# Performance work log

Hardware: AMD Instinct MI355X
Metric: run time of the kernel (lower is better)

## Reference

```python
import jax, jax.numpy as jnp
import numpy as np

B, S, H, TRK = 128, 256, 300, 64  # batch, seq tokens, hidden size, tracker size
N_STEPS = 2 * S - 1


def _valid_transitions(rng, batch, n_tok):
    """Random valid shift(0)/reduce(1) sequences of length 2*n_tok-1."""
    out = np.zeros((batch, 2 * n_tok - 1), dtype=np.int32)
    for b in range(batch):
        shifts_left, depth = n_tok, 0
        for i in range(2 * n_tok - 1):
            if depth < 2:
                a = 0
            elif shifts_left == 0:
                a = 1
            else:
                a = int(rng.integers(0, 2))
            out[b, i] = a
            if a == 0:
                shifts_left -= 1
                depth += 1
            else:
                depth -= 1
    return out


def setup_inputs() -> dict:
    key = jax.random.key(0)
    ks = jax.random.split(key, 12)
    sh = 1.0 / np.sqrt(H)
    st = 1.0 / np.sqrt(TRK)
    bufs = jax.random.normal(ks[0], (B, S, 2 * H), dtype=jnp.float32)
    transitions = jnp.asarray(_valid_transitions(np.random.default_rng(0), B, S))
    return {
        "bufs": bufs,
        "transitions": transitions,
        # tracker bundling projections (bias=False): Linear(size, 4*tracker)
        "W_buf": jax.random.uniform(ks[1], (H, 4 * TRK), jnp.float32, -sh, sh),
        "W_s1": jax.random.uniform(ks[2], (H, 4 * TRK), jnp.float32, -sh, sh),
        "W_s2": jax.random.uniform(ks[3], (H, 4 * TRK), jnp.float32, -sh, sh),
        # tracker LSTMCell(4*TRK, TRK, bias=False)
        "W_ih": jax.random.uniform(ks[4], (4 * TRK, 4 * TRK), jnp.float32, -st, st),
        "W_hh": jax.random.uniform(ks[5], (4 * TRK, TRK), jnp.float32, -st, st),
        # transition predictor Linear(TRK, 2)
        "W_trans": jax.random.uniform(ks[6], (TRK, 2), jnp.float32, -st, st),
        "b_trans": jax.random.uniform(ks[7], (2,), jnp.float32, -st, st),
        # Reduce (TreeLSTM composition, 5*H gates) with tracking input
        "W_left": jax.random.uniform(ks[8], (H, 5 * H), jnp.float32, -sh, sh),
        "W_right": jax.random.uniform(ks[9], (H, 5 * H), jnp.float32, -sh, sh),
        "W_track": jax.random.uniform(ks[10], (TRK, 5 * H), jnp.float32, -st, st),
        "b_reduce": jax.random.uniform(ks[11], (5 * H,), jnp.float32, -sh, sh),
    }


def reference(bufs, transitions, W_buf, W_s1, W_s2, W_ih, W_hh,
              W_trans, b_trans, W_left, W_right, W_track, b_reduce):
    Bn, Sn, D = bufs.shape
    Hn = D // 2  # element = concat(h, c)
    Tn = W_hh.shape[1]
    bidx = jnp.arange(Bn)

    stack0 = jnp.zeros((Bn, Sn + 1, D), dtype=bufs.dtype)
    carry0 = (stack0,
              jnp.zeros((Bn,), jnp.int32),          # stack ptr
              jnp.zeros((Bn,), jnp.int32),          # buffer ptr
              jnp.zeros((Bn, Tn), bufs.dtype),       # tracker h
              jnp.zeros((Bn, Tn), bufs.dtype))       # tracker c

    def gather(stack, ptr, off):
        el = stack[bidx, jnp.clip(ptr - off, 0)]
        return jnp.where((ptr >= off)[:, None], el, jnp.zeros_like(el))

    def step(carry, trans):
        stack, sptr, bptr, th, tc = carry
        buf_top = bufs[bidx, jnp.clip(bptr, 0, Sn - 1)]   # [B, 2H]
        s1 = gather(stack, sptr, 1)                        # stack[-1]
        s2 = gather(stack, sptr, 2)                        # stack[-2]
        # bundle h-parts -> tracker LSTM input (sum of three projections)
        lstm_in = buf_top[:, :Hn] @ W_buf + s1[:, :Hn] @ W_s1 + s2[:, :Hn] @ W_s2
        gates = lstm_in @ W_ih.T + th @ W_hh.T             # [B, 4T]
        gi, gf, gg, go = jnp.split(gates, 4, axis=1)       # torch LSTMCell order i,f,g,o
        tc = jax.nn.sigmoid(gf) * tc + jax.nn.sigmoid(gi) * jnp.tanh(gg)
        th = jax.nn.sigmoid(go) * jnp.tanh(tc)
        logits = th @ W_trans + b_trans                    # [B, 2]
        # TreeLSTM reduce: left = stack[-2], right = stack[-1]
        a = s2[:, :Hn] @ W_left + s1[:, :Hn] @ W_right + th @ W_track + b_reduce
        ri, fl, fr, ro, rg = jnp.split(a, 5, axis=1)
        rc = (jax.nn.sigmoid(fl) * s2[:, Hn:] + jax.nn.sigmoid(fr) * s1[:, Hn:]
              + jax.nn.sigmoid(ri) * jnp.tanh(rg))
        rh = jax.nn.sigmoid(ro) * jnp.tanh(rc)
        reduced = jnp.concatenate([rh, rc], axis=1)
        is_shift = (trans == 0)
        new_el = jnp.where(is_shift[:, None], buf_top, reduced)
        wpos = jnp.where(is_shift, sptr, jnp.clip(sptr - 2, 0))
        stack = stack.at[bidx, wpos].set(new_el)
        sptr = jnp.where(is_shift, sptr + 1, sptr - 1)
        bptr = bptr + is_shift.astype(jnp.int32)
        return (stack, sptr, bptr, th, tc), logits

    (stack, sptr, _, _, _), logits = jax.lax.scan(step, carry0, transitions.T)
    final_h = stack[bidx, jnp.clip(sptr - 1, 0)][:, :Hn]   # [B, H]
    # pack sentence encoding + per-step transition logits into one array
    return jnp.concatenate(
        [final_h, logits.transpose(1, 0, 2).reshape(Bn, -1)], axis=1)
```

## Files before the change

### kernel.cpp

```cpp
#include <hip/hip_runtime.h>


#define NSTEP 511
#define HB 128
#define SQ 256
#define HD 300
#define DW 600
#define TK 64

#define NB 16
#define NE 25
#define JPB 12
#define DOTS_E 60
#define KE 640
#define UPB 10
#define DOTS_T 40
#define KT2 1000
#define ASTR 20
#define SLP 820
#define OUTW 1322

#define N_WEB 960000
#define N_WTB 280000
#define N_WTR 97500
#define N_TH  16384
#define N_STACK 19660800
#define N_BAR 1024
#define N_TPK 4096
#define N_WCT 230400

#define OFF_WEB 0
#define OFF_WTB 960000
#define OFF_WTR 1240000
#define OFF_TH  1337504
#define OFF_STACK 1353888
#define OFF_BAR 21014688
#define OFF_TPK 21015712
#define WS_FLOATS 21019808
#define OFF_WCT OFF_STACK

#define L_ACT 0
#define L_DUMP 20500
#define EDP 964
#define TDP 644
#define L_WTR 28212
#define L_THL 32112
#define L_BRED 33152
#define L_TRW 36600
#define L_INT 37112
#define LDS_FLOATS 37208

__device__ __forceinline__ float sigf(float x) { return 1.0f / (1.0f + __expf(-x)); }

__global__ void prep_a(const float* __restrict__ Wbuf, const float* __restrict__ Ws1,
                       const float* __restrict__ Ws2, const int* __restrict__ trans,
                       float* __restrict__ ws) {
  int idx = blockIdx.x * 256 + threadIdx.x;
  if (idx < N_WCT) {
    int k = idx % 900;
    int m = idx / 900;
    float v = (k < 300) ? Wbuf[k*256 + m]
            : (k < 600) ? Ws1[(k-300)*256 + m]
                        : Ws2[(k-600)*256 + m];
    ws[OFF_WCT + idx] = v;
    return;
  }
  idx -= N_WCT;
  if (idx < N_TH) { ws[OFF_TH + idx] = 0.0f; return; }
  idx -= N_TH;
  if (idx < N_BAR) { ws[OFF_BAR + idx] = 0.0f; return; }
  idx -= N_BAR;
  if (idx < 8*NSTEP) {
    int g = idx / NSTEP, t = idx % NSTEP;
    int w = 0;
    #pragma unroll
    for (int b = 0; b < 16; ++b)
      w |= (trans[(size_t)(g*16 + b)*NSTEP + t] & 1) << b;
    ((int*)(ws + OFF_TPK))[g*NSTEP + t] = w;
  }
}

__global__ void prep_b(const float* __restrict__ Wih, const float* __restrict__ Whh,
                       const float* __restrict__ Wl, const float* __restrict__ Wr,
                       const float* __restrict__ Wtrk, float* __restrict__ ws) {
  int idx = blockIdx.x * 256 + threadIdx.x;
  if (idx < N_WEB) {
    int k = idx % KE; int rest = idx / KE;
    int dot = rest % DOTS_E; int e = rest / DOTS_E;
    int g = dot / JPB, jj = dot % JPB;
    int col = g*HD + e*JPB + jj;
    float v = 0.0f;
    if (k < 300)      v = Wl[k*1500 + col];
    else if (k < 600) v = Wr[(k-300)*1500 + col];
    ws[OFF_WEB + idx] = v;
    return;
  }
  idx -= N_WEB;
  if (idx < N_WTB) {
    int k = idx % KT2; int rest = idx / KT2;
    int dot = rest % DOTS_T; int tb = rest / DOTS_T;
    int g = dot / UPB, uu = dot % UPB;
    int ucnt = (tb == 6) ? 10 : 9;
    float v = 0.0f;
    if (uu < ucnt) {
      int col = g*TK + tb*9 + uu;
      if (k < 900) {
        const float* wct = ws + OFF_WCT;
        const float* wi  = Wih + col*256;
        float s = 0.0f;
        #pragma unroll 4
        for (int m = 0; m < 256; ++m) s = fmaf(wct[m*900 + k], wi[m], s);
        v = s;
      } else if (k < 964) {
        v = Whh[col*TK + (k - 900)];
      }
    }
    ws[OFF_WTB + idx] = v;
    return;
  }
  idx -= N_WTB;
  if (idx < N_WTR) {
    int k = idx % 65; int rest = idx / 65;
    int dot = rest % DOTS_E; int e = rest / DOTS_E;
    int g = dot / JPB, jj = dot % JPB;
    ws[OFF_WTR + idx] = (k < 64) ? Wtrk[k*1500 + (g*HD + e*JPB + jj)] : 0.0f;
  }
}

__device__ __forceinline__ void xbar(int role, unsigned epoch,
                                     volatile unsigned* slots, volatile unsigned* flag,
                                     volatile int* broken) {
  __syncthreads();
  if (role == 0) {
    if (threadIdx.x < 64) {
      int lane = threadIdx.x;
      unsigned spins = 0;
      for (;;) {
        if (*broken) break;
        unsigned v = (lane >= 1 && lane < 32) ? slots[lane] : epoch;
        if (__all(v >= epoch)) break;
        __builtin_amdgcn_s_sleep(1);
        asm volatile("buffer_inv" ::: "memory");
        if (++spins > 2000000u) { if (lane == 0) *broken = 1; break; }
      }
      if (lane == 0) {
        *flag = epoch;
        asm volatile("s_waitcnt vmcnt(0)" ::: "memory");
      }
    }
  } else if (threadIdx.x == 0) {
    slots[role] = epoch;
    asm volatile("s_waitcnt vmcnt(0)" ::: "memory");
    unsigned spins = 0;
    while (!*broken && *flag < epoch) {
      __builtin_amdgcn_s_sleep(1);
      asm volatile("buffer_inv" ::: "memory");
      if (++spins > 2000000u) *broken = 1;
    }
  }
  __syncthreads();
  asm volatile("buffer_inv" ::: "memory");
}

__launch_bounds__(256, 1)
__global__ void spinn_kernel(const float* __restrict__ bufs,
                             const float* __restrict__ Wtrans, const float* __restrict__ btrans,
                             const float* __restrict__ bredv,
                             float* __restrict__ ws, float* __restrict__ out) {
  extern __shared__ float lds[];
  int* ibuf = (int*)(lds + L_INT);
  int* redl = ibuf + 16;
  int* shl  = ibuf + 32;
  int* sptr = ibuf + 48;
  int* bptr = ibuf + 64;
  volatile int* broken = ibuf + 82;
  int* role_s = ibuf + 90;
  int* trw = (int*)(lds + L_TRW);

  const int tid = threadIdx.x;

  unsigned xcc;
  asm volatile("s_getreg_b32 %0, hwreg(HW_REG_XCC_ID)" : "=s"(xcc));
  xcc &= 7u;
  if (tid == 0) {
    unsigned slot = __hip_atomic_fetch_add((unsigned*)(ws + OFF_BAR) + 512 + xcc, 1u,
                                           __ATOMIC_RELAXED, __HIP_MEMORY_SCOPE_AGENT);
    *role_s = (int)slot;
    *broken = 0;
  }
  __syncthreads();
  const int role = *role_s;
  const int group = (int)xcc;
  if (role >= 32) return;

  const int b0 = group * NB;
  const bool isE = (role < NE);
  const int e  = role;
  const int tb = role - NE;
  const int u0 = (tb >= 0) ? tb*9 : 0;
  const int ucnt = (tb == 6) ? 10 : 9;

  volatile unsigned* slots = (volatile unsigned*)((unsigned*)(ws + OFF_BAR) + (size_t)group*64);
  volatile unsigned* flag  = slots + 32;

  float* stack = ws + OFF_STACK;
  float* thbuf = ws + OFF_TH;

  float tc_reg = 0.0f;

  float4 wreg[4][10];
  if (isE) {
    if (tid < 240) {
      const int q = tid >> 4, kq = tid & 15;
      const float* wb = ws + OFF_WEB;
      #pragma unroll
      for (int d = 0; d < 4; ++d)
        #pragma unroll
        for (int i = 0; i < 10; ++i)
          wreg[d][i] = *(const float4*)(wb + (size_t)(e*DOTS_E + 4*q + d)*KE + kq*40 + 4*i);
    }
  } else {
    if (tid < 250) {
      const int q = tid / 25, kq = tid % 25;
      const float* wb = ws + OFF_WTB;
      #pragma unroll
      for (int d = 0; d < 4; ++d)
        #pragma unroll
        for (int i = 0; i < 10; ++i)
          wreg[d][i] = *(const float4*)(wb + (size_t)(tb*DOTS_T + 4*q + d)*KT2 + kq*40 + 4*i);
    }
  }

  if (tid < 16) { sptr[tid] = 0; bptr[tid] = 0; }
  for (int i = tid; i < NSTEP; i += 256)
    trw[i] = ((const int*)(ws + OFF_TPK))[group*NSTEP + i];
  if (isE) {
    for (int i = tid; i < DOTS_E*65; i += 256)
      lds[L_WTR + i] = ws[OFF_WTR + (size_t)e*DOTS_E*65 + i];
    for (int i = tid; i < DOTS_E; i += 256)
      lds[L_BRED + i] = bredv[(i/JPB)*HD + e*JPB + (i%JPB)];
    for (int i = tid; i < 800; i += 256) lds[615*ASTR + i] = 0.0f;
  } else {
    for (int i = tid; i < 720; i += 256) lds[988*ASTR + i] = 0.0f;
  }
  __syncthreads();

  unsigned epoch = 0;

  for (int t = 0; t < NSTEP; ++t) {
    const int w = trw[t] & 0xFFFF;
    const int nred = __popc(w);
    if (tid < 16) {
      int rank = __popc(w & ((1u << tid) - 1u));
      if ((w >> tid) & 1) redl[rank] = tid; else shl[tid - rank] = tid;
    }
    __syncthreads();

    if (isE) {
      int r = tid >> 4, lane = tid & 15;
      if (r < nred) {
        int b = redl[r];
        int sp = sptr[b];
        const float* s2p = stack + ((size_t)((b0+b)*SQ + sp-2))*DW;
        const float* s1p = stack + ((size_t)((b0+b)*SQ + sp-1))*DW;
        #pragma unroll 4
        for (int i = 0; i < 10; ++i) {
          int ch = lane + 16*i;
          if (ch < 150) {
            int sec = ch / 75, kc = ch % 75;
            int dim = kc*4;
            const float* src = (sec == 0) ? s2p : s1p;
            float4 v = *(const float4*)(src + dim);
            int kbase = sec*300 + dim;
            int row0 = (kbase/40)*41 + (kbase%40);
            lds[(row0+0)*ASTR + r] = v.x;
            lds[(row0+1)*ASTR + r] = v.y;
            lds[(row0+2)*ASTR + r] = v.z;
            lds[(row0+3)*ASTR + r] = v.w;
          }
        }
      }
    } else {
      {
        int b = tid >> 4, lane = tid & 15;
        int bp = bptr[b]; if (bp > SQ-1) bp = SQ-1;
        int sp = sptr[b];
        const float* bsrc = bufs + ((size_t)((b0+b)*SQ + bp))*DW;
        const float* s1p = (sp >= 1) ? stack + ((size_t)((b0+b)*SQ + sp-1))*DW : nullptr;
        const float* s2p = (sp >= 2) ? stack + ((size_t)((b0+b)*SQ + sp-2))*DW : nullptr;
        #pragma unroll 4
        for (int i = 0; i < 15; ++i) {
          int ch = lane + 16*i;
          if (ch < 225) {
            int sec = ch / 75, kc = ch % 75;
            int dim = kc*4;
            const float* src = (sec == 0) ? bsrc : ((sec == 1) ? s1p : s2p);
            float4 v = make_float4(0.f, 0.f, 0.f, 0.f);
            if (src) v = *(const float4*)(src + dim);
            int kbase = sec*300 + dim;
            int row0 = (kbase/40)*41 + (kbase%40);
            lds[(row0+0)*ASTR + b] = v.x;
            lds[(row0+1)*ASTR + b] = v.y;
            lds[(row0+2)*ASTR + b] = v.z;
            lds[(row0+3)*ASTR + b] = v.w;
          }
        }
      }
      {
        int pm = (t - 1) & 1;
        int b = tid >> 4, uc = tid & 15;
        float4 v = *(const float4*)(thbuf + ((size_t)pm*HB + (b0+b))*TK + uc*4);
        float vv[4] = {v.x, v.y, v.z, v.w};
        #pragma unroll
        for (int l = 0; l < 4; ++l) {
          int k = 900 + uc*4 + l;
          int row = (k/40)*41 + (k%40);
          lds[row*ASTR + b] = vv[l];
        }
      }
    }
    __syncthreads();

    if (isE) {
      const int nchunk = (nred + 3) >> 2;
      if (nchunk > 0) {
        if (tid < 240) {
          const int q = tid >> 4, kq = tid & 15;
          const float* ab = lds + kq*SLP;
          float* dmp = lds + L_DUMP;
          #pragma unroll 1
          for (int c = 0; c < nchunk; ++c) {
            float acc[4][4];
            #pragma unroll
            for (int d = 0; d < 4; ++d)
              #pragma unroll
              for (int s = 0; s < 4; ++s) acc[d][s] = 0.0f;
            #pragma unroll
            for (int i = 0; i < 10; ++i) {
              #pragma unroll
              for (int kk = 0; kk < 4; ++kk) {
                float4 a = *(const float4*)(ab + (4*i + kk)*ASTR + 4*c);
                #pragma unroll
                for (int d = 0; d < 4; ++d) {
                  float wv = (kk == 0) ? wreg[d][i].x : (kk == 1) ? wreg[d][i].y
                           : (kk == 2) ? wreg[d][i].z : wreg[d][i].w;
                  acc[d][0] = fmaf(wv, a.x, acc[d][0]);
                  acc[d][1] = fmaf(wv, a.y, acc[d][1]);
                  acc[d][2] = fmaf(wv, a.z, acc[d][2]);
                  acc[d][3] = fmaf(wv, a.w, acc[d][3]);
                }
              }
            }
            #pragma unroll
            for (int d = 0; d < 4; ++d)
              #pragma unroll
              for (int s = 0; s < 4; ++s)
                acc[d][s] += __shfl_xor(acc[d][s], 8, 64);
            if (kq < 8) {
              #pragma unroll
              for (int d = 0; d < 4; ++d)
                *(float4*)(dmp + kq*EDP + (4*q + d)*16 + 4*c) =
                    make_float4(acc[d][0], acc[d][1], acc[d][2], acc[d][3]);
            }
          }
        }
        __syncthreads();
        for (int task = tid; task < DOTS_E*16; task += 256) {
          int dot = task >> 4, s = task & 15;
          float sum = 0.0f;
          #pragma unroll
          for (int kq = 0; kq < 8; ++kq)
            sum += lds[L_DUMP + kq*EDP + dot*16 + s];
          lds[L_DUMP + dot*16 + s] = sum;
        }
      }
    } else {
      if (tid < 250) {
        const int q = tid / 25, kq = tid % 25;
        const float* ab = lds + kq*SLP;
        float* dmp = lds + L_DUMP + kq*TDP;
        #pragma unroll 1
        for (int c = 0; c < 4; ++c) {
          float acc[4][4];
          #pragma unroll
          for (int d = 0; d < 4; ++d)
            #pragma unroll
            for (int s = 0; s < 4; ++s) acc[d][s] = 0.0f;
          #pragma unroll
          for (int i = 0; i < 10; ++i) {
            #pragma unroll
            for (int kk = 0; kk < 4; ++kk) {
              float4 a = *(const float4*)(ab + (4*i + kk)*ASTR + 4*c);
              #pragma unroll
              for (int d = 0; d < 4; ++d) {
                float wv = (kk == 0) ? wreg[d][i].x : (kk == 1) ? wreg[d][i].y
                         : (kk == 2) ? wreg[d][i].z : wreg[d][i].w;
                acc[d][0] = fmaf(wv, a.x, acc[d][0]);
                acc[d][1] = fmaf(wv, a.y, acc[d][1]);
                acc[d][2] = fmaf(wv, a.z, acc[d][2]);
                acc[d][3] = fmaf(wv, a.w, acc[d][3]);
              }
            }
          }
          #pragma unroll
          for (int d = 0; d < 4; ++d)
            *(float4*)(dmp + (4*q + d)*16 + 4*c) =
                make_float4(acc[d][0], acc[d][1], acc[d][2], acc[d][3]);
        }
      }
      __syncthreads();
      for (int task = tid; task < DOTS_T*16; task += 256) {
        int dot = task >> 4, s = task & 15;
        float sum = 0.0f;
        #pragma unroll
        for (int kq = 0; kq < 25; ++kq)
          sum += lds[L_DUMP + kq*TDP + dot*16 + s];
        lds[L_DUMP + dot*16 + s] = sum;
      }
      __syncthreads();
      if (tid < 160) {
        int uu = tid >> 4, b = tid & 15;
        if (uu < ucnt) {
          float gi = lds[L_DUMP + (0*UPB + uu)*16 + b];
          float gf = lds[L_DUMP + (1*UPB + uu)*16 + b];
          float gg = lds[L_DUMP + (2*UPB + uu)*16 + b];
          float go = lds[L_DUMP + (3*UPB + uu)*16 + b];
          tc_reg = sigf(gf)*tc_reg + sigf(gi)*tanhf(gg);
          float th = sigf(go)*tanhf(tc_reg);
          thbuf[((size_t)(t & 1)*HB + (b0 + b))*TK + (u0 + uu)] = th;
        }
      }
    }

    ++epoch;
    xbar(role, epoch, slots, flag, broken);

    if (isE) {
      int p = t & 1;
      {
        int r = tid >> 4, lane = tid & 15;
        if (r < nred) {
          const float* thp = thbuf + ((size_t)p*HB + (b0 + redl[r]))*TK;
          #pragma unroll
          for (int i = 0; i < 4; ++i) {
            int k = lane + 16*i;
            lds[L_THL + r*65 + k] = thp[k];
          }
        }
      }
      __syncthreads();
      if (tid < 192) {
        int rr = tid / JPB, jj = tid % JPB;
        int j = e*JPB + jj;
        if (rr < nred) {
          int b = redl[rr];
          int sp = sptr[b];
          float* s2base = stack + ((size_t)((b0+b)*SQ + (sp-2)))*DW;
          const float* s1base = stack + ((size_t)((b0+b)*SQ + (sp-1)))*DW;
          float s2c = s2base[HD + j];
          float s1c = s1base[HD + j];
          float a0 = lds[L_DUMP + (0*JPB + jj)*16 + rr] + lds[L_BRED + 0*JPB + jj];
          float a1 = lds[L_DUMP + (1*JPB + jj)*16 + rr] + lds[L_BRED + 1*JPB + jj];
          float a2 = lds[L_DUMP + (2*JPB + jj)*16 + rr] + lds[L_BRED + 2*JPB + jj];
          float a3 = lds[L_DUMP + (3*JPB + jj)*16 + rr] + lds[L_BRED + 3*JPB + jj];
          float a4 = lds[L_DUMP + (4*JPB + jj)*16 + rr] + lds[L_BRED + 4*JPB + jj];
          #pragma unroll 8
          for (int k = 0; k < 64; ++k) {
            float tv = lds[L_THL + rr*65 + k];
            a0 = fmaf(tv, lds[L_WTR + (0*JPB + jj)*65 + k], a0);
            a1 = fmaf(tv, lds[L_WTR + (1*JPB + jj)*65 + k], a1);
            a2 = fmaf(tv, lds[L_WTR + (2*JPB + jj)*65 + k], a2);
            a3 = fmaf(tv, lds[L_WTR + (3*JPB + jj)*65 + k], a3);
            a4 = fmaf(tv, lds[L_WTR + (4*JPB + jj)*65 + k], a4);
          }
          float rc = sigf(a1)*s2c + sigf(a2)*s1c + sigf(a0)*tanhf(a4);
          float rh = sigf(a3)*tanhf(rc);
          s2base[j] = rh;
          s2base[HD + j] = rc;
        } else {
          int b = shl[rr - nred];
          int sp = sptr[b], bp = bptr[b];
          const float* src = bufs + ((size_t)((b0+b)*SQ + bp))*DW;
          float* dst = stack + ((size_t)((b0+b)*SQ + sp))*DW;
          dst[j] = src[j];
          dst[HD + j] = src[HD + j];
        }
      }
    } else if (role == NE) {
      if (tid < 32) {
        int b = tid >> 1, c = tid & 1;
        const float* th = thbuf + ((size_t)(t & 1)*HB + (b0 + b))*TK;
        float s = btrans[c];
        #pragma unroll 8
        for (int u = 0; u < TK; ++u) s = fmaf(th[u], Wtrans[u*2 + c], s);
        out[(size_t)(b0 + b)*OUTW + HD + 2*t + c] = s;
      }
    }

    __syncthreads();
    if (tid < 16) {
      if (!((w >> tid) & 1)) { sptr[tid] += 1; bptr[tid] += 1; }
      else                   { sptr[tid] -= 1; }
    }

    ++epoch;
    xbar(role, epoch, slots, flag, broken);
  }

  if (isE && tid < 192) {
    int b = tid / JPB, jj = tid % JPB;
    int j = e*JPB + jj;
    int sp = sptr[b] - 1; if (sp < 0) sp = 0;
    out[(size_t)(b0 + b)*OUTW + j] =
        stack[((size_t)((b0 + b)*SQ + sp))*DW + j];
  }
}

extern "C" void kernel_launch(void* const* d_in, const int* in_sizes, int n_in,
                              void* d_out, int out_size, void* d_ws, size_t ws_size,
                              hipStream_t stream) {
  const float* bufs   = (const float*)d_in[0];
  const int*   trans  = (const int*)  d_in[1];
  const float* Wbuf   = (const float*)d_in[2];
  const float* Ws1    = (const float*)d_in[3];
  const float* Ws2    = (const float*)d_in[4];
  const float* Wih    = (const float*)d_in[5];
  const float* Whh    = (const float*)d_in[6];
  const float* Wtrans = (const float*)d_in[7];
  const float* btrans = (const float*)d_in[8];
  const float* Wl     = (const float*)d_in[9];
  const float* Wr     = (const float*)d_in[10];
  const float* Wtrk   = (const float*)d_in[11];
  const float* bredv  = (const float*)d_in[12];
  float* ws  = (float*)d_ws;
  float* out = (float*)d_out;

  if (ws_size < (size_t)WS_FLOATS * sizeof(float)) return;

  {
    int total = N_WCT + N_TH + N_BAR + 8*NSTEP;
    prep_a<<<(total + 255) / 256, 256, 0, stream>>>(Wbuf, Ws1, Ws2, trans, ws);
  }
  {
    int total = N_WEB + N_WTB + N_WTR;
    prep_b<<<(total + 255) / 256, 256, 0, stream>>>(Wih, Whh, Wl, Wr, Wtrk, ws);
  }
  (void)hipFuncSetAttribute((const void*)spinn_kernel,
                            hipFuncAttributeMaxDynamicSharedMemorySize, 160000);
  spinn_kernel<<<256, 256, LDS_FLOATS * sizeof(float), stream>>>(
      bufs, Wtrans, btrans, bredv, ws, out);
}
```

Baseline: 13.02 ms.

## Quadruple threads per block and spread dot products across more lanes

Raises the block size from 256 to 1024 threads. Each thread now holds one weight row slice instead of four, so the per-step matvec has four times the threads, each running a shorter dependency chain with fewer registers. The tracker-input reduction in the reduce phase is split across four lanes with shuffle reductions, and the staging loads use wider lanes. The aim is lower per-step latency in this latency-bound recurrent loop, at the cost of more wavefronts in each __syncthreads and the cross-block barrier, and the launch-bounds change affects register allocation.

```diff
diff --git a/kernel.cpp b/kernel.cpp
--- a/kernel.cpp
+++ b/kernel.cpp
@@ -162,7 +162,7 @@
   asm volatile("buffer_inv" ::: "memory");
 }
 
-__launch_bounds__(256, 1)
+__launch_bounds__(1024, 4)
 __global__ void spinn_kernel(const float* __restrict__ bufs,
                              const float* __restrict__ Wtrans, const float* __restrict__ btrans,
                              const float* __restrict__ bredv,
@@ -208,40 +208,34 @@
 
   float tc_reg = 0.0f;
 
-  float4 wreg[4][10];
+  float4 wreg[10];
   if (isE) {
-    if (tid < 240) {
+    if (tid < 960) {
       const int q = tid >> 4, kq = tid & 15;
-      const float* wb = ws + OFF_WEB;
+      const float* wb = ws + OFF_WEB + (size_t)(e*DOTS_E + q)*KE + kq*40;
       #pragma unroll
-      for (int d = 0; d < 4; ++d)
-        #pragma unroll
-        for (int i = 0; i < 10; ++i)
-          wreg[d][i] = *(const float4*)(wb + (size_t)(e*DOTS_E + 4*q + d)*KE + kq*40 + 4*i);
+      for (int i = 0; i < 10; ++i) wreg[i] = *(const float4*)(wb + 4*i);
     }
   } else {
-    if (tid < 250) {
+    if (tid < 1000) {
       const int q = tid / 25, kq = tid % 25;
-      const float* wb = ws + OFF_WTB;
+      const float* wb = ws + OFF_WTB + (size_t)(tb*DOTS_T + q)*KT2 + kq*40;
       #pragma unroll
-      for (int d = 0; d < 4; ++d)
-        #pragma unroll
-        for (int i = 0; i < 10; ++i)
-          wreg[d][i] = *(const float4*)(wb + (size_t)(tb*DOTS_T + 4*q + d)*KT2 + kq*40 + 4*i);
+      for (int i = 0; i < 10; ++i) wreg[i] = *(const float4*)(wb + 4*i);
     }
   }
 
   if (tid < 16) { sptr[tid] = 0; bptr[tid] = 0; }
-  for (int i = tid; i < NSTEP; i += 256)
+  for (int i = tid; i < NSTEP; i += 1024)
     trw[i] = ((const int*)(ws + OFF_TPK))[group*NSTEP + i];
   if (isE) {
-    for (int i = tid; i < DOTS_E*65; i += 256)
+    for (int i = tid; i < DOTS_E*65; i += 1024)
       lds[L_WTR + i] = ws[OFF_WTR + (size_t)e*DOTS_E*65 + i];
-    for (int i = tid; i < DOTS_E; i += 256)
+    for (int i = tid; i < DOTS_E; i += 1024)
       lds[L_BRED + i] = bredv[(i/JPB)*HD + e*JPB + (i%JPB)];
-    for (int i = tid; i < 800; i += 256) lds[615*ASTR + i] = 0.0f;
+    for (int i = tid; i < 800; i += 1024) lds[615*ASTR + i] = 0.0f;
   } else {
-    for (int i = tid; i < 720; i += 256) lds[988*ASTR + i] = 0.0f;
+    for (int i = tid; i < 720; i += 1024) lds[988*ASTR + i] = 0.0f;
   }
   __syncthreads();
 
@@ -257,15 +251,15 @@
     __syncthreads();
 
     if (isE) {
-      int r = tid >> 4, lane = tid & 15;
+      int r = tid >> 6, lane = tid & 63;
       if (r < nred) {
         int b = redl[r];
         int sp = sptr[b];
         const float* s2p = stack + ((size_t)((b0+b)*SQ + sp-2))*DW;
         const float* s1p = stack + ((size_t)((b0+b)*SQ + sp-1))*DW;
-        #pragma unroll 4
-        for (int i = 0; i < 10; ++i) {
-          int ch = lane + 16*i;
+        #pragma unroll
+        for (int i = 0; i < 3; ++i) {
+          int ch = lane + 64*i;
           if (ch < 150) {
             int sec = ch / 75, kc = ch % 75;
             int dim = kc*4;
@@ -282,15 +276,15 @@
       }
     } else {
       {
-        int b = tid >> 4, lane = tid & 15;
+        int b = tid >> 6, lane = tid & 63;
         int bp = bptr[b]; if (bp > SQ-1) bp = SQ-1;
         int sp = sptr[b];
         const float* bsrc = bufs + ((size_t)((b0+b)*SQ + bp))*DW;
         const float* s1p = (sp >= 1) ? stack + ((size_t)((b0+b)*SQ + sp-1))*DW : nullptr;
         const float* s2p = (sp >= 2) ? stack + ((size_t)((b0+b)*SQ + sp-2))*DW : nullptr;
-        #pragma unroll 4
-        for (int i = 0; i < 15; ++i) {
-          int ch = lane + 16*i;
+        #pragma unroll
+        for (int i = 0; i < 4; ++i) {
+          int ch = lane + 64*i;
           if (ch < 225) {
             int sec = ch / 75, kc = ch % 75;
             int dim = kc*4;
@@ -306,7 +300,7 @@
           }
         }
       }
-      {
+      if (tid < 256) {
         int pm = (t - 1) & 1;
         int b = tid >> 4, uc = tid & 15;
         float4 v = *(const float4*)(thbuf + ((size_t)pm*HB + (b0+b))*TK + uc*4);
@@ -324,48 +318,36 @@
     if (isE) {
       const int nchunk = (nred + 3) >> 2;
       if (nchunk > 0) {
-        if (tid < 240) {
+        if (tid < 960) {
           const int q = tid >> 4, kq = tid & 15;
           const float* ab = lds + kq*SLP;
           float* dmp = lds + L_DUMP;
           #pragma unroll 1
           for (int c = 0; c < nchunk; ++c) {
-            float acc[4][4];
-            #pragma unroll
-            for (int d = 0; d < 4; ++d)
-              #pragma unroll
-              for (int s = 0; s < 4; ++s) acc[d][s] = 0.0f;
+            float a0 = 0.f, a1 = 0.f, a2 = 0.f, a3 = 0.f;
             #pragma unroll
             for (int i = 0; i < 10; ++i) {
               #pragma unroll
               for (int kk = 0; kk < 4; ++kk) {
                 float4 a = *(const float4*)(ab + (4*i + kk)*ASTR + 4*c);
-                #pragma unroll
-                for (int d = 0; d < 4; ++d) {
-                  float wv = (kk == 0) ? wreg[d][i].x : (kk == 1) ? wreg[d][i].y
-                           : (kk == 2) ? wreg[d][i].z : wreg[d][i].w;
-                  acc[d][0] = fmaf(wv, a.x, acc[d][0]);
-                  acc[d][1] = fmaf(wv, a.y, acc[d][1]);
-                  acc[d][2] = fmaf(wv, a.z, acc[d][2]);
-                  acc[d][3] = fmaf(wv, a.w, acc[d][3]);
-                }
+                float wv = (kk == 0) ? wreg[i].x : (kk == 1) ? wreg[i].y
+                         : (kk == 2) ? wreg[i].z : wreg[i].w;
+                a0 = fmaf(wv, a.x, a0);
+                a1 = fmaf(wv, a.y, a1);
+                a2 = fmaf(wv, a.z, a2);
+                a3 = fmaf(wv, a.w, a3);
               }
             }
-            #pragma unroll
-            for (int d = 0; d < 4; ++d)
-              #pragma unroll
-              for (int s = 0; s < 4; ++s)
-                acc[d][s] += __shfl_xor(acc[d][s], 8, 64);
-            if (kq < 8) {
-              #pragma unroll
-              for (int d = 0; d < 4; ++d)
-                *(float4*)(dmp + kq*EDP + (4*q + d)*16 + 4*c) =
-                    make_float4(acc[d][0], acc[d][1], acc[d][2], acc[d][3]);
-            }
+            a0 += __shfl_xor(a0, 8, 64);
+            a1 += __shfl_xor(a1, 8, 64);
+            a2 += __shfl_xor(a2, 8, 64);
+            a3 += __shfl_xor(a3, 8, 64);
+            if (kq < 8)
+              *(float4*)(dmp + kq*EDP + q*16 + 4*c) = make_float4(a0, a1, a2, a3);
           }
         }
         __syncthreads();
-        for (int task = tid; task < DOTS_E*16; task += 256) {
+        for (int task = tid; task < DOTS_E*16; task += 1024) {
           int dot = task >> 4, s = task & 15;
           float sum = 0.0f;
           #pragma unroll
@@ -375,41 +357,31 @@
         }
       }
     } else {
-      if (tid < 250) {
+      if (tid < 1000) {
         const int q = tid / 25, kq = tid % 25;
         const float* ab = lds + kq*SLP;
         float* dmp = lds + L_DUMP + kq*TDP;
         #pragma unroll 1
         for (int c = 0; c < 4; ++c) {
-          float acc[4][4];
-          #pragma unroll
-          for (int d = 0; d < 4; ++d)
-            #pragma unroll
-            for (int s = 0; s < 4; ++s) acc[d][s] = 0.0f;
+          float a0 = 0.f, a1 = 0.f, a2 = 0.f, a3 = 0.f;
           #pragma unroll
           for (int i = 0; i < 10; ++i) {
             #pragma unroll
             for (int kk = 0; kk < 4; ++kk) {
               float4 a = *(const float4*)(ab + (4*i + kk)*ASTR + 4*c);
-              #pragma unroll
-              for (int d = 0; d < 4; ++d) {
-                float wv = (kk == 0) ? wreg[d][i].x : (kk == 1) ? wreg[d][i].y
-                         : (kk == 2) ? wreg[d][i].z : wreg[d][i].w;
-                acc[d][0] = fmaf(wv, a.x, acc[d][0]);
-                acc[d][1] = fmaf(wv, a.y, acc[d][1]);
-                acc[d][2] = fmaf(wv, a.z, acc[d][2]);
-                acc[d][3] = fmaf(wv, a.w, acc[d][3]);
-              }
+              float wv = (kk == 0) ? wreg[i].x : (kk == 1) ? wreg[i].y
+                       : (kk == 2) ? wreg[i].z : wreg[i].w;
+              a0 = fmaf(wv, a.x, a0);
+              a1 = fmaf(wv, a.y, a1);
+              a2 = fmaf(wv, a.z, a2);
+              a3 = fmaf(wv, a.w, a3);
             }
           }
-          #pragma unroll
-          for (int d = 0; d < 4; ++d)
-            *(float4*)(dmp + (4*q + d)*16 + 4*c) =
-                make_float4(acc[d][0], acc[d][1], acc[d][2], acc[d][3]);
+          *(float4*)(dmp + q*16 + 4*c) = make_float4(a0, a1, a2, a3);
         }
       }
       __syncthreads();
-      for (int task = tid; task < DOTS_T*16; task += 256) {
+      for (int task = tid; task < DOTS_T*16; task += 1024) {
         int dot = task >> 4, s = task & 15;
         float sum = 0.0f;
         #pragma unroll
@@ -437,7 +409,7 @@
 
     if (isE) {
       int p = t & 1;
-      {
+      if (tid < 256) {
         int r = tid >> 4, lane = tid & 15;
         if (r < nred) {
           const float* thp = thbuf + ((size_t)p*HB + (b0 + redl[r]))*TK;
@@ -449,41 +421,56 @@
         }
       }
       __syncthreads();
-      if (tid < 192) {
-        int rr = tid / JPB, jj = tid % JPB;
+      if (tid < 768) {
+        int rr = tid / 48, rem = tid % 48;
+        int jj = rem >> 2, ks = rem & 3;
         int j = e*JPB + jj;
         if (rr < nred) {
           int b = redl[rr];
           int sp = sptr[b];
           float* s2base = stack + ((size_t)((b0+b)*SQ + (sp-2)))*DW;
           const float* s1base = stack + ((size_t)((b0+b)*SQ + (sp-1)))*DW;
-          float s2c = s2base[HD + j];
-          float s1c = s1base[HD + j];
-          float a0 = lds[L_DUMP + (0*JPB + jj)*16 + rr] + lds[L_BRED + 0*JPB + jj];
-          float a1 = lds[L_DUMP + (1*JPB + jj)*16 + rr] + lds[L_BRED + 1*JPB + jj];
-          float a2 = lds[L_DUMP + (2*JPB + jj)*16 + rr] + lds[L_BRED + 2*JPB + jj];
-          float a3 = lds[L_DUMP + (3*JPB + jj)*16 + rr] + lds[L_BRED + 3*JPB + jj];
-          float a4 = lds[L_DUMP + (4*JPB + jj)*16 + rr] + lds[L_BRED + 4*JPB + jj];
-          #pragma unroll 8
-          for (int k = 0; k < 64; ++k) {
-            float tv = lds[L_THL + rr*65 + k];
-            a0 = fmaf(tv, lds[L_WTR + (0*JPB + jj)*65 + k], a0);
-            a1 = fmaf(tv, lds[L_WTR + (1*JPB + jj)*65 + k], a1);
-            a2 = fmaf(tv, lds[L_WTR + (2*JPB + jj)*65 + k], a2);
-            a3 = fmaf(tv, lds[L_WTR + (3*JPB + jj)*65 + k], a3);
-            a4 = fmaf(tv, lds[L_WTR + (4*JPB + jj)*65 + k], a4);
-          }
-          float rc = sigf(a1)*s2c + sigf(a2)*s1c + sigf(a0)*tanhf(a4);
-          float rh = sigf(a3)*tanhf(rc);
-          s2base[j] = rh;
-          s2base[HD + j] = rc;
+          float a0 = 0.f, a1 = 0.f, a2 = 0.f, a3 = 0.f, a4 = 0.f;
+          const float* thl = lds + L_THL + rr*65 + ks*16;
+          const float* w0 = lds + L_WTR + (0*JPB + jj)*65 + ks*16;
+          const float* w1 = lds + L_WTR + (1*JPB + jj)*65 + ks*16;
+          const float* w2 = lds + L_WTR + (2*JPB + jj)*65 + ks*16;
+          const float* w3 = lds + L_WTR + (3*JPB + jj)*65 + ks*16;
+          const float* w4 = lds + L_WTR + (4*JPB + jj)*65 + ks*16;
+          #pragma unroll
+          for (int k = 0; k < 16; ++k) {
+            float tv = thl[k];
+            a0 = fmaf(tv, w0[k], a0);
+            a1 = fmaf(tv, w1[k], a1);
+            a2 = fmaf(tv, w2[k], a2);
+            a3 = fmaf(tv, w3[k], a3);
+            a4 = fmaf(tv, w4[k], a4);
+          }
+          a0 += __shfl_xor(a0, 1, 64); a0 += __shfl_xor(a0, 2, 64);
+          a1 += __shfl_xor(a1, 1, 64); a1 += __shfl_xor(a1, 2, 64);
+          a2 += __shfl_xor(a2, 1, 64); a2 += __shfl_xor(a2, 2, 64);
+          a3 += __shfl_xor(a3, 1, 64); a3 += __shfl_xor(a3, 2, 64);
+          a4 += __shfl_xor(a4, 1, 64); a4 += __shfl_xor(a4, 2, 64);
+          if (ks == 0) {
+            a0 += lds[L_DUMP + (0*JPB + jj)*16 + rr] + lds[L_BRED + 0*JPB + jj];
+            a1 += lds[L_DUMP + (1*JPB + jj)*16 + rr] + lds[L_BRED + 1*JPB + jj];
+            a2 += lds[L_DUMP + (2*JPB + jj)*16 + rr] + lds[L_BRED + 2*JPB + jj];
+            a3 += lds[L_DUMP + (3*JPB + jj)*16 + rr] + lds[L_BRED + 3*JPB + jj];
+            a4 += lds[L_DUMP + (4*JPB + jj)*16 + rr] + lds[L_BRED + 4*JPB + jj];
+            float s2c = s2base[HD + j];
+            float s1c = s1base[HD + j];
+            float rc = sigf(a1)*s2c + sigf(a2)*s1c + sigf(a0)*tanhf(a4);
+            float rh = sigf(a3)*tanhf(rc);
+            s2base[j] = rh;
+            s2base[HD + j] = rc;
+          }
         } else {
           int b = shl[rr - nred];
           int sp = sptr[b], bp = bptr[b];
           const float* src = bufs + ((size_t)((b0+b)*SQ + bp))*DW;
           float* dst = stack + ((size_t)((b0+b)*SQ + sp))*DW;
-          dst[j] = src[j];
-          dst[HD + j] = src[HD + j];
+          if (ks == 0) dst[j] = src[j];
+          else if (ks == 1) dst[HD + j] = src[HD + j];
         }
       }
     } else if (role == NE) {
@@ -547,6 +534,6 @@
   }
   (void)hipFuncSetAttribute((const void*)spinn_kernel,
                             hipFuncAttributeMaxDynamicSharedMemorySize, 160000);
-  spinn_kernel<<<256, 256, LDS_FLOATS * sizeof(float), stream>>>(
+  spinn_kernel<<<256, 1024, LDS_FLOATS * sizeof(float), stream>>>(
       bufs, Wtrans, btrans, bredv, ws, out);
 }
```

Measured after the change: 19.37 ms. +48.7%, slower.
